# Kernel optimization log

Measured on AMD Instinct MI355X. Metric: run time of the kernel, lower is better.

Reference implementation:

```python
import jax, jax.numpy as jnp
import numpy as np

D = 512      # hidden_size
H = 8        # num_heads
EPS = 1e-5   # torch LayerNorm default eps


def _ln(x, g, b):
    m = x.mean(-1, keepdims=True)
    v = ((x - m) ** 2).mean(-1, keepdims=True)
    return (x - m) * jax.lax.rsqrt(v + EPS) * g + b


def _xavier(k, shape):
    fan_in, fan_out = shape
    lim = (6.0 / (fan_in + fan_out)) ** 0.5
    return jax.random.uniform(k, shape, jnp.float32, -lim, lim)


def setup_inputs() -> dict:
    key = jax.random.key(0)
    ks = jax.random.split(key, 8)
    lengths = np.array([512, 640, 768, 896, 1024, 512, 768, 1024], dtype=np.int64)
    cum = np.concatenate([np.zeros(1, np.int64), np.cumsum(lengths)])  # [9], last = 6144
    T = int(cum[-1])
    return {
        "h_n": jax.random.normal(ks[0], (T, D), jnp.float32),
        "to_v_w": _xavier(ks[1], (D, D)), "to_v_b": jnp.zeros((D,), jnp.float32),
        "to_qk_w": _xavier(ks[2], (D, 2 * D)), "to_qk_b": jnp.zeros((2 * D,), jnp.float32),
        "proj_w": _xavier(ks[3], (D, D)), "proj_b": jnp.zeros((D,), jnp.float32),
        "ffn_w1": _xavier(ks[4], (D, 4 * D)), "ffn_b1": jnp.zeros((4 * D,), jnp.float32),
        "ffn_w2": _xavier(ks[5], (4 * D, D)), "ffn_b2": jnp.zeros((D,), jnp.float32),
        "ln1_g": jnp.ones((D,), jnp.float32), "ln1_b": jnp.zeros((D,), jnp.float32),
        "ln2_g": jnp.ones((D,), jnp.float32), "ln2_b": jnp.zeros((D,), jnp.float32),
        "num_query_cumsum": jnp.asarray(cum),
    }


def reference(h_n, to_v_w, to_v_b, to_qk_w, to_qk_b, proj_w, proj_b,
              ffn_w1, ffn_b1, ffn_w2, ffn_b2, ln1_g, ln1_b, ln2_g, ln2_b,
              num_query_cumsum):
    # --- static ragged layout (indices are constants) ---
    cum = np.asarray(num_query_cumsum)
    lengths = np.diff(cum)                       # [B]
    B = int(lengths.size)
    N = int(lengths.max())                       # max_num_nodes
    T = int(cum[-1])
    bid = np.repeat(np.arange(B), lengths)       # [T] graph id per token
    pos = np.arange(T) - cum[bid]                # [T] slot within graph
    pad_mask = np.arange(N)[None, :] >= lengths[:, None]  # [B, N], True = padding

    hd = D // H
    scale = hd ** -0.5

    # --- projections on the flat ragged tokens ---
    v = h_n @ to_v_w + to_v_b                    # [T, D]
    qk = h_n @ to_qk_w + to_qk_b                 # [T, 2D]
    q, k = qk[:, :D], qk[:, D:]

    # --- pad ragged -> dense [B, H, N, hd] ---
    def pad(x):
        xp = jnp.zeros((B, N, D), x.dtype).at[bid, pos].set(x)
        return xp.reshape(B, N, H, hd).transpose(0, 2, 1, 3)

    qp, kp, vp = pad(q), pad(k), pad(v)

    # --- dense masked softmax attention (keys masked at pad slots) ---
    scores = jnp.einsum('bhnd,bhmd->bhnm', qp, kp) * scale
    scores = jnp.where(pad_mask[:, None, None, :], -jnp.inf, scores)
    attn = jax.nn.softmax(scores, axis=-1)
    ctx = jnp.einsum('bhnm,bhmd->bhnd', attn, vp)

    # --- unpad back to flat [T, D] ---
    h_new = ctx.transpose(0, 2, 1, 3).reshape(B, N, D)[bid, pos]

    # --- residual + LN + FFN + LN (dropout = 0) ---
    h1 = _ln(h_n + (h_new @ proj_w + proj_b), ln1_g, ln1_b)
    ffn = jax.nn.gelu(h1 @ ffn_w1 + ffn_b1, approximate=False) @ ffn_w2 + ffn_b2
    return _ln(h1 + ffn, ln2_g, ln2_b)
```

## Files before the change

kernel.cpp:

```cpp
#include <hip/hip_runtime.h>

typedef __bf16 bf16;
typedef __bf16 bf16x8 __attribute__((ext_vector_type(8)));
typedef __bf16 bf16x4 __attribute__((ext_vector_type(4)));
typedef float  f32x4  __attribute__((ext_vector_type(4)));

#define MFMA16 __builtin_amdgcn_mfma_f32_16x16x32_bf16

__device__ __forceinline__ void gl2lds16(const bf16* g, bf16* l) {
  __builtin_amdgcn_global_load_lds(
      (const __attribute__((address_space(1))) unsigned int*)g,
      (__attribute__((address_space(3))) unsigned int*)l, 16, 0, 0);
}

__device__ __forceinline__ int dt_bf16(const void* g1) {
  return (((const unsigned*)g1)[0] == 0x3F800000u) ? 0 : 1;
}
__device__ __forceinline__ float load_any(const void* p, int i, int f) {
  return f ? (float)((const bf16*)p)[i] : ((const float*)p)[i];
}

__global__ __launch_bounds__(256) void prep_all(
    const void* __restrict__ h, const void* __restrict__ w_qk,
    const void* __restrict__ w_v, const void* __restrict__ w_pr,
    const void* __restrict__ w_f1, const void* __restrict__ w_f2,
    const void* __restrict__ b_qk, const void* __restrict__ b_v,
    const void* __restrict__ b_pr, const void* __restrict__ b_f1,
    const void* __restrict__ b_f2, const void* __restrict__ g1,
    const void* __restrict__ b1, const void* __restrict__ g2,
    const void* __restrict__ b2,
    bf16* __restrict__ hb, bf16* __restrict__ Wtqkv, bf16* __restrict__ Wtpr,
    bf16* __restrict__ Wtf1, bf16* __restrict__ Wtf2,
    float* __restrict__ vec, int T) {
  __shared__ bf16 tile[32][33];
  const int f = dt_bf16(g1);
  const int t = threadIdx.x;
  int b = blockIdx.x;
  const int HB = (T * 512) / 2048;

  if (b < HB) {
    const int i = (b * 256 + t) * 8;
    if (f) {
      *(bf16x8*)&hb[i] = *(const bf16x8*)((const bf16*)h + i);
    } else {
      const float* hf = (const float*)h;
      bf16x8 v;
#pragma unroll
      for (int j = 0; j < 8; j++) v[j] = (bf16)hf[i + j];
      *(bf16x8*)&hb[i] = v;
    }
    return;
  }
  b -= HB;

  if (b < 3072) {
    const void* in; bf16* out; int K, N;
    if (b < 512)       { in = w_qk; out = Wtqkv;                     K = 512;  N = 1024; }
    else if (b < 768)  { b -= 512;  in = w_v;  out = Wtqkv + (size_t)1024 * 512; K = 512; N = 512; }
    else if (b < 1024) { b -= 768;  in = w_pr; out = Wtpr;           K = 512;  N = 512; }
    else if (b < 2048) { b -= 1024; in = w_f1; out = Wtf1;           K = 512;  N = 2048; }
    else               { b -= 2048; in = w_f2; out = Wtf2;           K = 2048; N = 512; }
    const int tilesx = N / 32;
    const int bx = (b % tilesx) * 32, by = (b / tilesx) * 32;
    const int tx = t & 31, ty = t >> 5;
#pragma unroll
    for (int i = 0; i < 32; i += 8)
      tile[ty + i][tx] = (bf16)load_any(in, (by + ty + i) * N + bx + tx, f);
    __syncthreads();
#pragma unroll
    for (int i = 0; i < 32; i += 8)
      out[(size_t)(bx + ty + i) * K + by + tx] = tile[tx][ty + i];
    return;
  }
  b -= 3072;

  const int i = b * 256 + t;
  if (i >= 6656) return;
  const void* src; int base;
  if (i < 1024)      { src = b_qk; base = 0; }
  else if (i < 1536) { src = b_v;  base = 1024; }
  else if (i < 2048) { src = b_pr; base = 1536; }
  else if (i < 4096) { src = b_f1; base = 2048; }
  else if (i < 4608) { src = b_f2; base = 4096; }
  else if (i < 5120) { src = g1;   base = 4608; }
  else if (i < 5632) { src = b1;   base = 5120; }
  else if (i < 6144) { src = g2;   base = 5632; }
  else               { src = b2;   base = 6144; }
  vec[i] = load_any(src, i - base, f);
}

template <int BM, int MODE>
__global__ __launch_bounds__(256) void gemm_lds(const bf16* __restrict__ A,
                                                const bf16* __restrict__ Bt,
                                                const float* __restrict__ bias,
                                                void* __restrict__ aux,
                                                void* __restrict__ outp,
                                                void* __restrict__ outp2,
                                                int N, int K, int ldA, int ldB,
                                                int ldT) {
  constexpr int BN = 128;
  constexpr int WAVES_M = BM / 64;
  constexpr int WAVES_N = 4 / WAVES_M;
  constexpr int WN = BN / WAVES_N;
  constexpr int NI = WN / 16;
  __shared__ __align__(16) bf16 As[BM * 64];
  __shared__ __align__(16) bf16 Bs[BN * 64];
  const int t = threadIdx.x;
  const int m0 = blockIdx.x * BM, n0 = blockIdx.y * BN;
  const int lane = t & 63, wv = t >> 6;
  const int wm = (wv / WAVES_N) * 64;
  const int wn = (wv % WAVES_N) * WN;
  const int qd = lane >> 4, cl = lane & 15;
  const int koff = (MODE == 6) ? blockIdx.z * K : 0;

  const f32x4 fz = {0.f, 0.f, 0.f, 0.f};
  f32x4 acc[4][NI];
#pragma unroll
  for (int i = 0; i < 4; i++)
#pragma unroll
    for (int j = 0; j < NI; j++) acc[i][j] = fz;

  const int srow = wv * 8 + (lane >> 3);
  const int sch = (lane & 7) ^ (lane >> 3);
  const bf16* pA = A + (size_t)(m0 + srow) * ldA + koff + sch * 8;
  const bf16* pB = Bt + (size_t)(n0 + srow) * ldB + koff + sch * 8;
  bf16* AsW = As + wv * 8 * 64;
  bf16* BsW = Bs + wv * 8 * 64;

  for (int k0 = 0; k0 < K; k0 += 64) {
    __syncthreads();
#pragma unroll
    for (int op = 0; op < BM / 32; op++)
      gl2lds16(pA + (size_t)(op * 32) * ldA, AsW + op * 32 * 64);
#pragma unroll
    for (int op = 0; op < 4; op++)
      gl2lds16(pB + (size_t)(op * 32) * ldB, BsW + op * 32 * 64);
    pA += 64; pB += 64;
    __syncthreads();

#pragma unroll
    for (int ss = 0; ss < 2; ss++) {
      bf16x8 af[4], bfr[NI];
#pragma unroll
      for (int i = 0; i < 4; i++)
        af[i] = *(const bf16x8*)&As[(wm + i * 16 + cl) * 64 +
                                    ((ss * 4 + qd) ^ (cl & 7)) * 8];
#pragma unroll
      for (int i = 0; i < NI; i++)
        bfr[i] = *(const bf16x8*)&Bs[(wn + i * 16 + cl) * 64 +
                                     ((ss * 4 + qd) ^ (cl & 7)) * 8];
#pragma unroll
      for (int mi = 0; mi < 4; mi++)
#pragma unroll
        for (int ni = 0; ni < NI; ni++)
          acc[mi][ni] = MFMA16(af[mi], bfr[ni], acc[mi][ni], 0, 0, 0);
    }
  }

  float bv[NI];
#pragma unroll
  for (int ni = 0; ni < NI; ni++)
    bv[ni] = (MODE == 6) ? 0.f : bias[n0 + wn + ni * 16 + cl];

#pragma unroll
  for (int mi = 0; mi < 4; mi++) {
    const int mbase = m0 + wm + mi * 16 + qd * 4;
#pragma unroll
    for (int ni = 0; ni < NI; ni++) {
      const int n = n0 + wn + ni * 16 + cl;
      if (MODE == 5) {
        if (n0 < 1024) {
          bf16* out = (bf16*)outp;
#pragma unroll
          for (int r = 0; r < 4; r++)
            out[(size_t)(mbase + r) * 1024 + n] = (bf16)(acc[mi][ni][r] + bv[ni]);
        } else {
          bf16* vtp = (bf16*)aux;
          bf16x4 pk;
#pragma unroll
          for (int r = 0; r < 4; r++) pk[r] = (bf16)(acc[mi][ni][r] + bv[ni]);
          *(bf16x4*)&vtp[(size_t)(n - 1024) * ldT + mbase] = pk;
        }
      } else if (MODE == 2) {
        float* out = (float*)outp;
        const bf16* res = (const bf16*)aux;
#pragma unroll
        for (int r = 0; r < 4; r++)
          out[(size_t)(mbase + r) * N + n] =
              acc[mi][ni][r] + bv[ni] + (float)res[(size_t)(mbase + r) * N + n];
      } else if (MODE == 3) {
        bf16* out = (bf16*)outp;
#pragma unroll
        for (int r = 0; r < 4; r++) {
          float x = acc[mi][ni][r] + bv[ni];
          float gl = 0.5f * x * (1.0f + erff(x * 0.70710678118654752f));
          out[(size_t)(mbase + r) * N + n] = (bf16)gl;
        }
      } else {
        float* out = (float*)(blockIdx.z ? outp2 : outp);
#pragma unroll
        for (int r = 0; r < 4; r++)
          out[(size_t)(mbase + r) * N + n] = acc[mi][ni][r];
      }
    }
  }
}

__global__ __launch_bounds__(256) void attn_kernel(const bf16* __restrict__ qk,
                                                   const bf16* __restrict__ vt,
                                                   bf16* __restrict__ ctx,
                                                   const int* __restrict__ cumraw,
                                                   int T, int ncum) {
  __shared__ __align__(16) bf16 Ks[2][64 * 64];
  __shared__ __align__(16) bf16 Vs[2][64 * 64];
  __shared__ __align__(16) bf16 P[4][16 * 64];
  const int wv = threadIdx.x >> 6, lane = threadIdx.x & 63;
  const int qd = lane >> 4, cl = lane & 15;
  const int q0b = blockIdx.x * 64;
  const int q0 = q0b + wv * 16;
  const int h = blockIdx.y;

  const int stride = (cumraw[1] == 0) ? 2 : 1;
  int kstart = 0, kend = T;
  for (int i = 1; i < ncum; i++) {
    int c = cumraw[i * stride];
    if (c > q0b) { kend = c; break; }
    kstart = c;
  }

  const bf16* qbase = qk + (size_t)(q0 + cl) * 1024 + h * 64 + qd * 8;
  bf16x8 qf0 = *(const bf16x8*)qbase;
  bf16x8 qf1 = *(const bf16x8*)(qbase + 32);

  const f32x4 fz = {0.f, 0.f, 0.f, 0.f};
  f32x4 o[4] = {fz, fz, fz, fz};
  float lacc[4] = {0.f, 0.f, 0.f, 0.f};

  const int srow = wv * 8 + (lane >> 3);
  const int schunk = (lane & 7) ^ (srow & 7);
  const bf16* kg = qk + 512 + (size_t)h * 64 + schunk * 8;
  const bf16* vg = vt + (size_t)(h * 64 + srow) * T + schunk * 8;
  const int woff = wv * 8 * 64;

  const int bch = qd ^ (cl & 7);
  const float cc = 0.1803368801111204f;

  {
    const bf16* kg0 = kg + (size_t)(kstart + srow) * 1024;
    gl2lds16(kg0, Ks[0] + woff);
    gl2lds16(kg0 + (size_t)32 * 1024, Ks[0] + woff + 32 * 64);
    const bf16* vg0 = vg + kstart;
    gl2lds16(vg0, Vs[0] + woff);
    gl2lds16(vg0 + (size_t)32 * T, Vs[0] + woff + 32 * 64);
  }

  int ib = 0;
  for (int kc = kstart; kc < kend; kc += 64, ib ^= 1) {
    __syncthreads();

    if (kc + 64 < kend) {
      const bf16* kg0 = kg + (size_t)(kc + 64 + srow) * 1024;
      gl2lds16(kg0, Ks[ib ^ 1] + woff);
      gl2lds16(kg0 + (size_t)32 * 1024, Ks[ib ^ 1] + woff + 32 * 64);
      const bf16* vg0 = vg + kc + 64;
      gl2lds16(vg0, Vs[ib ^ 1] + woff);
      gl2lds16(vg0 + (size_t)32 * T, Vs[ib ^ 1] + woff + 32 * 64);
    }

    f32x4 s[4];
#pragma unroll
    for (int ni = 0; ni < 4; ni++) {
      const bf16* kr = Ks[ib] + (ni * 16 + cl) * 64;
      f32x4 tacc = fz;
      tacc = MFMA16(qf0, *(const bf16x8*)(kr + bch * 8), tacc, 0, 0, 0);
      tacc = MFMA16(qf1, *(const bf16x8*)(kr + (bch ^ 4) * 8), tacc, 0, 0, 0);
      s[ni] = tacc;
    }

    bf16* Pw = P[wv];
#pragma unroll
    for (int r = 0; r < 4; r++) {
      const float p0 = __builtin_amdgcn_exp2f(s[0][r] * cc);
      const float p1 = __builtin_amdgcn_exp2f(s[1][r] * cc);
      const float p2 = __builtin_amdgcn_exp2f(s[2][r] * cc);
      const float p3 = __builtin_amdgcn_exp2f(s[3][r] * cc);
      lacc[r] += (p0 + p1) + (p2 + p3);
      const int prow = qd * 4 + r;
      const int px = prow & 7;
      const int cb = cl >> 3, ci = cl & 7;
      Pw[prow * 64 + ((cb ^ px) * 8) + ci] = (bf16)p0;
      Pw[prow * 64 + (((2 + cb) ^ px) * 8) + ci] = (bf16)p1;
      Pw[prow * 64 + (((4 + cb) ^ px) * 8) + ci] = (bf16)p2;
      Pw[prow * 64 + (((6 + cb) ^ px) * 8) + ci] = (bf16)p3;
    }

    const int pch = qd ^ (cl & 7);
    const bf16* pr = Pw + cl * 64;
    bf16x8 pf0 = *(const bf16x8*)(pr + pch * 8);
    bf16x8 pf1 = *(const bf16x8*)(pr + (pch ^ 4) * 8);
#pragma unroll
    for (int dt = 0; dt < 4; dt++) {
      const bf16* vr = Vs[ib] + (dt * 16 + cl) * 64;
      o[dt] = MFMA16(pf0, *(const bf16x8*)(vr + bch * 8), o[dt], 0, 0, 0);
      o[dt] = MFMA16(pf1, *(const bf16x8*)(vr + (bch ^ 4) * 8), o[dt], 0, 0, 0);
    }
  }

  float linv[4];
#pragma unroll
  for (int r = 0; r < 4; r++) {
    float l = lacc[r];
    l += __shfl_xor(l, 1);
    l += __shfl_xor(l, 2);
    l += __shfl_xor(l, 4);
    l += __shfl_xor(l, 8);
    linv[r] = __builtin_amdgcn_rcpf(l);
  }
#pragma unroll
  for (int dt = 0; dt < 4; dt++) {
#pragma unroll
    for (int r = 0; r < 4; r++) {
      float y = o[dt][r] * linv[r];
      ctx[(size_t)(q0 + qd * 4 + r) * 512 + h * 64 + dt * 16 + cl] = (bf16)y;
    }
  }
}

__global__ __launch_bounds__(256) void ln_kernel(const float* __restrict__ s,
                                                 const float* __restrict__ g,
                                                 const float* __restrict__ b,
                                                 bf16* __restrict__ outb) {
  const int row = blockIdx.x * 4 + (threadIdx.x >> 6);
  const int lane = threadIdx.x & 63;
  const float4* sr = (const float4*)(s + (size_t)row * 512);
  float4 x0 = sr[lane];
  float4 x1 = sr[lane + 64];
  float sum = x0.x + x0.y + x0.z + x0.w + x1.x + x1.y + x1.z + x1.w;
  float sq = x0.x * x0.x + x0.y * x0.y + x0.z * x0.z + x0.w * x0.w +
             x1.x * x1.x + x1.y * x1.y + x1.z * x1.z + x1.w * x1.w;
#pragma unroll
  for (int off = 1; off < 64; off <<= 1) {
    sum += __shfl_xor(sum, off);
    sq += __shfl_xor(sq, off);
  }
  const float mean = sum * (1.0f / 512.0f);
  const float var = sq * (1.0f / 512.0f) - mean * mean;
  const float rs = rsqrtf(var + 1e-5f);
  const float4* gp = (const float4*)g;
  const float4* bp = (const float4*)b;
  float4 g0 = gp[lane], g1v = gp[lane + 64];
  float4 b0 = bp[lane], b1v = bp[lane + 64];
  float xv[8] = {x0.x, x0.y, x0.z, x0.w, x1.x, x1.y, x1.z, x1.w};
  float gv[8] = {g0.x, g0.y, g0.z, g0.w, g1v.x, g1v.y, g1v.z, g1v.w};
  float bb[8] = {b0.x, b0.y, b0.z, b0.w, b1v.x, b1v.y, b1v.z, b1v.w};
  bf16x4 o0, o1;
#pragma unroll
  for (int j = 0; j < 4; j++) {
    o0[j] = (bf16)((xv[j] - mean) * rs * gv[j] + bb[j]);
    o1[j] = (bf16)((xv[4 + j] - mean) * rs * gv[4 + j] + bb[4 + j]);
  }
  *(bf16x4*)&outb[(size_t)row * 512 + lane * 4] = o0;
  *(bf16x4*)&outb[(size_t)row * 512 + 256 + lane * 4] = o1;
}

__global__ __launch_bounds__(256) void ln2_kernel(const float* __restrict__ s2a,
                                                  const float* __restrict__ s2b,
                                                  const bf16* __restrict__ h1b,
                                                  const float* __restrict__ bias,
                                                  const float* __restrict__ g,
                                                  const float* __restrict__ b,
                                                  void* __restrict__ outb,
                                                  const void* __restrict__ g1probe) {
  const int row = blockIdx.x * 4 + (threadIdx.x >> 6);
  const int lane = threadIdx.x & 63;
  const float4* sa = (const float4*)(s2a + (size_t)row * 512);
  const float4* sb = (const float4*)(s2b + (size_t)row * 512);
  const float4* bi = (const float4*)bias;
  float4 a0 = sa[lane], a1 = sa[lane + 64];
  float4 c0 = sb[lane], c1 = sb[lane + 64];
  float4 v0 = bi[lane], v1 = bi[lane + 64];
  bf16x4 h0 = *(const bf16x4*)&h1b[(size_t)row * 512 + lane * 4];
  bf16x4 h1 = *(const bf16x4*)&h1b[(size_t)row * 512 + 256 + lane * 4];
  float x[8];
#pragma unroll
  for (int j = 0; j < 4; j++) {
    x[j] = (&a0.x)[j] + (&c0.x)[j] + (&v0.x)[j] + (float)h0[j];
    x[4 + j] = (&a1.x)[j] + (&c1.x)[j] + (&v1.x)[j] + (float)h1[j];
  }
  float sum = 0.f, sq = 0.f;
#pragma unroll
  for (int j = 0; j < 8; j++) { sum += x[j]; sq += x[j] * x[j]; }
#pragma unroll
  for (int off = 1; off < 64; off <<= 1) {
    sum += __shfl_xor(sum, off);
    sq += __shfl_xor(sq, off);
  }
  const float mean = sum * (1.0f / 512.0f);
  const float var = sq * (1.0f / 512.0f) - mean * mean;
  const float rs = rsqrtf(var + 1e-5f);
  const float4* gp = (const float4*)g;
  const float4* bp = (const float4*)b;
  float4 g0 = gp[lane], g1v = gp[lane + 64];
  float4 b0 = bp[lane], b1v = bp[lane + 64];
  float gv[8] = {g0.x, g0.y, g0.z, g0.w, g1v.x, g1v.y, g1v.z, g1v.w};
  float bb[8] = {b0.x, b0.y, b0.z, b0.w, b1v.x, b1v.y, b1v.z, b1v.w};
  float y[8];
#pragma unroll
  for (int j = 0; j < 8; j++) y[j] = (x[j] - mean) * rs * gv[j] + bb[j];

  if (dt_bf16(g1probe)) {
    bf16* ob = (bf16*)outb;
    bf16x4 o0, o1;
#pragma unroll
    for (int j = 0; j < 4; j++) { o0[j] = (bf16)y[j]; o1[j] = (bf16)y[4 + j]; }
    *(bf16x4*)&ob[(size_t)row * 512 + lane * 4] = o0;
    *(bf16x4*)&ob[(size_t)row * 512 + 256 + lane * 4] = o1;
  } else {
    float4* of = (float4*)((float*)outb + (size_t)row * 512);
    of[lane] = make_float4(y[0], y[1], y[2], y[3]);
    of[lane + 64] = make_float4(y[4], y[5], y[6], y[7]);
  }
}

extern "C" void kernel_launch(void* const* d_in, const int* in_sizes, int n_in,
                              void* d_out, int out_size, void* d_ws, size_t ws_size,
                              hipStream_t stream) {
  (void)n_in; (void)out_size; (void)ws_size;
  const void* h_n  = d_in[0];
  const void* w_v  = d_in[1];
  const void* b_v  = d_in[2];
  const void* w_qk = d_in[3];
  const void* b_qk = d_in[4];
  const void* w_pr = d_in[5];
  const void* b_pr = d_in[6];
  const void* w_f1 = d_in[7];
  const void* b_f1 = d_in[8];
  const void* w_f2 = d_in[9];
  const void* b_f2 = d_in[10];
  const void* g1w  = d_in[11];
  const void* b1w  = d_in[12];
  const void* g2w  = d_in[13];
  const void* b2w  = d_in[14];
  const int* cum   = (const int*)d_in[15];
  const int T = in_sizes[0] / 512;
  const int ncum = in_sizes[15];

  char* ws = (char*)d_ws;
  size_t off = 0;
  auto alloc = [&](size_t bytes) {
    char* p = ws + off;
    off += (bytes + 255) & ~(size_t)255;
    return p;
  };
  float* vec = (float*)alloc(6656 * 4);
  bf16* hb   = (bf16*)alloc((size_t)T * 512 * 2);
  bf16* qkb  = (bf16*)alloc((size_t)T * 1024 * 2);
  bf16* vt   = (bf16*)alloc((size_t)T * 512 * 2);
  bf16* ctx  = (bf16*)alloc((size_t)T * 512 * 2);
  float* s1  = (float*)alloc((size_t)T * 512 * 4);
  bf16* h1b  = (bf16*)alloc((size_t)T * 512 * 2);
  float* s2b = (float*)alloc((size_t)T * 512 * 4);
  bf16* Wtqkv = (bf16*)alloc((size_t)1536 * 512 * 2);
  bf16* Wtpr  = (bf16*)alloc((size_t)512 * 512 * 2);
  bf16* Wtf1  = (bf16*)alloc((size_t)2048 * 512 * 2);
  bf16* Wtf2  = (bf16*)alloc((size_t)512 * 2048 * 2);
  bf16* gbuf = qkb;
  float* s2a = s1;

  float* fb_qkv = vec + 0;
  float* fb_pr  = vec + 1536;
  float* fb_f1  = vec + 2048;
  float* fb_f2  = vec + 4096;
  float* fg1 = vec + 4608, *fb1 = vec + 5120;
  float* fg2 = vec + 5632, *fb2 = vec + 6144;

  const int prep_blocks = (T * 512) / 2048 + 3072 + 26;
  prep_all<<<prep_blocks, 256, 0, stream>>>(
      h_n, w_qk, w_v, w_pr, w_f1, w_f2,
      b_qk, b_v, b_pr, b_f1, b_f2, g1w, b1w, g2w, b2w,
      hb, Wtqkv, Wtpr, Wtf1, Wtf2, vec, T);

  gemm_lds<128, 5><<<dim3(T / 128, 12), 256, 0, stream>>>(
      hb, Wtqkv, fb_qkv, vt, qkb, nullptr, 1536, 512, 512, 512, T);
  attn_kernel<<<dim3(T / 64, 8), 256, 0, stream>>>(qkb, vt, ctx, cum, T, ncum);
  gemm_lds<64, 2><<<dim3(T / 64, 4), 256, 0, stream>>>(
      ctx, Wtpr, fb_pr, (void*)hb, s1, nullptr, 512, 512, 512, 512, 0);
  ln_kernel<<<T / 4, 256, 0, stream>>>(s1, fg1, fb1, h1b);
  gemm_lds<128, 3><<<dim3(T / 128, 16), 256, 0, stream>>>(
      h1b, Wtf1, fb_f1, nullptr, gbuf, nullptr, 2048, 512, 512, 512, 0);
  gemm_lds<128, 6><<<dim3(T / 128, 4, 2), 256, 0, stream>>>(
      gbuf, Wtf2, nullptr, nullptr, s2a, s2b, 512, 1024, 2048, 2048, 0);
  ln2_kernel<<<T / 4, 256, 0, stream>>>(s2a, s2b, h1b, fb_f2, fg2, fb2, d_out, g1w);
}
```

Baseline: 219.4 us.

## Process 32 queries per wave in attention; drop split-K for FFN2 GEMM

The attention kernel now gives each wave 32 query rows (two 16-row tiles) and each block 128 queries. Every K/V fragment read from LDS therefore feeds twice as many MFMAs, and the block count halves. Blocks that straddle a graph boundary load the union of key ranges, and each wave skips chunks outside its own graph. The FFN down-projection drops its split-K with two fp32 partial outputs and instead uses a single 64-row GEMM that fuses bias and residual, so ln2 reads only one buffer. The cost is fewer attention blocks, fewer FFN2 blocks with a longer K loop, and wasted K/V loads on boundary-straddling blocks.

```diff
diff --git a/kernel.cpp b/kernel.cpp
--- a/kernel.cpp
+++ b/kernel.cpp
@@ -95,7 +95,6 @@
                                                 const float* __restrict__ bias,
                                                 void* __restrict__ aux,
                                                 void* __restrict__ outp,
-                                                void* __restrict__ outp2,
                                                 int N, int K, int ldA, int ldB,
                                                 int ldT) {
   constexpr int BN = 128;
@@ -111,7 +110,6 @@
   const int wm = (wv / WAVES_N) * 64;
   const int wn = (wv % WAVES_N) * WN;
   const int qd = lane >> 4, cl = lane & 15;
-  const int koff = (MODE == 6) ? blockIdx.z * K : 0;
 
   const f32x4 fz = {0.f, 0.f, 0.f, 0.f};
   f32x4 acc[4][NI];
@@ -122,8 +120,8 @@
 
   const int srow = wv * 8 + (lane >> 3);
   const int sch = (lane & 7) ^ (lane >> 3);
-  const bf16* pA = A + (size_t)(m0 + srow) * ldA + koff + sch * 8;
-  const bf16* pB = Bt + (size_t)(n0 + srow) * ldB + koff + sch * 8;
+  const bf16* pA = A + (size_t)(m0 + srow) * ldA + sch * 8;
+  const bf16* pB = Bt + (size_t)(n0 + srow) * ldB + sch * 8;
   bf16* AsW = As + wv * 8 * 64;
   bf16* BsW = Bs + wv * 8 * 64;
 
@@ -159,8 +157,7 @@
 
   float bv[NI];
 #pragma unroll
-  for (int ni = 0; ni < NI; ni++)
-    bv[ni] = (MODE == 6) ? 0.f : bias[n0 + wn + ni * 16 + cl];
+  for (int ni = 0; ni < NI; ni++) bv[ni] = bias[n0 + wn + ni * 16 + cl];
 
 #pragma unroll
   for (int mi = 0; mi < 4; mi++) {
@@ -188,7 +185,7 @@
         for (int r = 0; r < 4; r++)
           out[(size_t)(mbase + r) * N + n] =
               acc[mi][ni][r] + bv[ni] + (float)res[(size_t)(mbase + r) * N + n];
-      } else if (MODE == 3) {
+      } else {
         bf16* out = (bf16*)outp;
 #pragma unroll
         for (int r = 0; r < 4; r++) {
@@ -196,11 +193,6 @@
           float gl = 0.5f * x * (1.0f + erff(x * 0.70710678118654752f));
           out[(size_t)(mbase + r) * N + n] = (bf16)gl;
         }
-      } else {
-        float* out = (float*)(blockIdx.z ? outp2 : outp);
-#pragma unroll
-        for (int r = 0; r < 4; r++)
-          out[(size_t)(mbase + r) * N + n] = acc[mi][ni][r];
       }
     }
   }
@@ -213,28 +205,42 @@
                                                    int T, int ncum) {
   __shared__ __align__(16) bf16 Ks[2][64 * 64];
   __shared__ __align__(16) bf16 Vs[2][64 * 64];
-  __shared__ __align__(16) bf16 P[4][16 * 64];
+  __shared__ __align__(16) bf16 P[4][32 * 64];
   const int wv = threadIdx.x >> 6, lane = threadIdx.x & 63;
   const int qd = lane >> 4, cl = lane & 15;
-  const int q0b = blockIdx.x * 64;
-  const int q0 = q0b + wv * 16;
+  const int q0b = blockIdx.x * 128;
+  const int q0w = q0b + wv * 32;
   const int h = blockIdx.y;
 
   const int stride = (cumraw[1] == 0) ? 2 : 1;
-  int kstart = 0, kend = T;
+  int ks_w = 0, ke_w = T;
   for (int i = 1; i < ncum; i++) {
     int c = cumraw[i * stride];
-    if (c > q0b) { kend = c; break; }
-    kstart = c;
-  }
-
-  const bf16* qbase = qk + (size_t)(q0 + cl) * 1024 + h * 64 + qd * 8;
-  bf16x8 qf0 = *(const bf16x8*)qbase;
-  bf16x8 qf1 = *(const bf16x8*)(qbase + 32);
+    if (c > q0w) { ke_w = c; break; }
+    ks_w = c;
+  }
+  int ks_u = 0, ke_u = T;
+  for (int i = 1; i < ncum; i++) {
+    int c = cumraw[i * stride];
+    if (c > q0b) { ke_u = c; break; }
+    ks_u = c;
+  }
+  for (int i = 1; i < ncum; i++) {
+    int c = cumraw[i * stride];
+    if (c > q0b + 127) { ke_u = c; break; }
+  }
+
+  bf16x8 qf[2][2];
+#pragma unroll
+  for (int a = 0; a < 2; a++) {
+    const bf16* qb = qk + (size_t)(q0w + a * 16 + cl) * 1024 + h * 64 + qd * 8;
+    qf[a][0] = *(const bf16x8*)qb;
+    qf[a][1] = *(const bf16x8*)(qb + 32);
+  }
 
   const f32x4 fz = {0.f, 0.f, 0.f, 0.f};
-  f32x4 o[4] = {fz, fz, fz, fz};
-  float lacc[4] = {0.f, 0.f, 0.f, 0.f};
+  f32x4 o[2][4] = {{fz, fz, fz, fz}, {fz, fz, fz, fz}};
+  float lacc[2][4] = {{0.f, 0.f, 0.f, 0.f}, {0.f, 0.f, 0.f, 0.f}};
 
   const int srow = wv * 8 + (lane >> 3);
   const int schunk = (lane & 7) ^ (srow & 7);
@@ -246,19 +252,19 @@
   const float cc = 0.1803368801111204f;
 
   {
-    const bf16* kg0 = kg + (size_t)(kstart + srow) * 1024;
+    const bf16* kg0 = kg + (size_t)(ks_u + srow) * 1024;
     gl2lds16(kg0, Ks[0] + woff);
     gl2lds16(kg0 + (size_t)32 * 1024, Ks[0] + woff + 32 * 64);
-    const bf16* vg0 = vg + kstart;
+    const bf16* vg0 = vg + ks_u;
     gl2lds16(vg0, Vs[0] + woff);
     gl2lds16(vg0 + (size_t)32 * T, Vs[0] + woff + 32 * 64);
   }
 
   int ib = 0;
-  for (int kc = kstart; kc < kend; kc += 64, ib ^= 1) {
+  for (int kc = ks_u; kc < ke_u; kc += 64, ib ^= 1) {
     __syncthreads();
 
-    if (kc + 64 < kend) {
+    if (kc + 64 < ke_u) {
       const bf16* kg0 = kg + (size_t)(kc + 64 + srow) * 1024;
       gl2lds16(kg0, Ks[ib ^ 1] + woff);
       gl2lds16(kg0 + (size_t)32 * 1024, Ks[ib ^ 1] + woff + 32 * 64);
@@ -267,61 +273,81 @@
       gl2lds16(vg0 + (size_t)32 * T, Vs[ib ^ 1] + woff + 32 * 64);
     }
 
-    f32x4 s[4];
-#pragma unroll
-    for (int ni = 0; ni < 4; ni++) {
-      const bf16* kr = Ks[ib] + (ni * 16 + cl) * 64;
-      f32x4 tacc = fz;
-      tacc = MFMA16(qf0, *(const bf16x8*)(kr + bch * 8), tacc, 0, 0, 0);
-      tacc = MFMA16(qf1, *(const bf16x8*)(kr + (bch ^ 4) * 8), tacc, 0, 0, 0);
-      s[ni] = tacc;
+    if (kc >= ks_w && kc < ke_w) {
+      f32x4 s[2][4];
+#pragma unroll
+      for (int ni = 0; ni < 4; ni++) {
+        const bf16* kr = Ks[ib] + (ni * 16 + cl) * 64;
+        bf16x8 k0 = *(const bf16x8*)(kr + bch * 8);
+        bf16x8 k1 = *(const bf16x8*)(kr + (bch ^ 4) * 8);
+#pragma unroll
+        for (int a = 0; a < 2; a++) {
+          f32x4 ta = fz;
+          ta = MFMA16(qf[a][0], k0, ta, 0, 0, 0);
+          ta = MFMA16(qf[a][1], k1, ta, 0, 0, 0);
+          s[a][ni] = ta;
+        }
+      }
+
+      bf16* Pw = P[wv];
+#pragma unroll
+      for (int a = 0; a < 2; a++) {
+        bf16* Pa = Pw + a * 16 * 64;
+#pragma unroll
+        for (int r = 0; r < 4; r++) {
+          const float p0 = __builtin_amdgcn_exp2f(s[a][0][r] * cc);
+          const float p1 = __builtin_amdgcn_exp2f(s[a][1][r] * cc);
+          const float p2 = __builtin_amdgcn_exp2f(s[a][2][r] * cc);
+          const float p3 = __builtin_amdgcn_exp2f(s[a][3][r] * cc);
+          lacc[a][r] += (p0 + p1) + (p2 + p3);
+          const int prow = qd * 4 + r;
+          const int px = prow & 7;
+          const int cb = cl >> 3, ci = cl & 7;
+          Pa[prow * 64 + ((cb ^ px) * 8) + ci] = (bf16)p0;
+          Pa[prow * 64 + (((2 + cb) ^ px) * 8) + ci] = (bf16)p1;
+          Pa[prow * 64 + (((4 + cb) ^ px) * 8) + ci] = (bf16)p2;
+          Pa[prow * 64 + (((6 + cb) ^ px) * 8) + ci] = (bf16)p3;
+        }
+      }
+
+      const int pch = qd ^ (cl & 7);
+      bf16x8 pf[2][2];
+#pragma unroll
+      for (int a = 0; a < 2; a++) {
+        const bf16* pr = Pw + a * 16 * 64 + cl * 64;
+        pf[a][0] = *(const bf16x8*)(pr + pch * 8);
+        pf[a][1] = *(const bf16x8*)(pr + (pch ^ 4) * 8);
+      }
+#pragma unroll
+      for (int dt = 0; dt < 4; dt++) {
+        const bf16* vr = Vs[ib] + (dt * 16 + cl) * 64;
+        bf16x8 v0 = *(const bf16x8*)(vr + bch * 8);
+        bf16x8 v1 = *(const bf16x8*)(vr + (bch ^ 4) * 8);
+#pragma unroll
+        for (int a = 0; a < 2; a++) {
+          o[a][dt] = MFMA16(pf[a][0], v0, o[a][dt], 0, 0, 0);
+          o[a][dt] = MFMA16(pf[a][1], v1, o[a][dt], 0, 0, 0);
+        }
+      }
     }
-
-    bf16* Pw = P[wv];
+  }
+
+#pragma unroll
+  for (int a = 0; a < 2; a++) {
 #pragma unroll
     for (int r = 0; r < 4; r++) {
-      const float p0 = __builtin_amdgcn_exp2f(s[0][r] * cc);
-      const float p1 = __builtin_amdgcn_exp2f(s[1][r] * cc);
-      const float p2 = __builtin_amdgcn_exp2f(s[2][r] * cc);
-      const float p3 = __builtin_amdgcn_exp2f(s[3][r] * cc);
-      lacc[r] += (p0 + p1) + (p2 + p3);
-      const int prow = qd * 4 + r;
-      const int px = prow & 7;
-      const int cb = cl >> 3, ci = cl & 7;
-      Pw[prow * 64 + ((cb ^ px) * 8) + ci] = (bf16)p0;
-      Pw[prow * 64 + (((2 + cb) ^ px) * 8) + ci] = (bf16)p1;
-      Pw[prow * 64 + (((4 + cb) ^ px) * 8) + ci] = (bf16)p2;
-      Pw[prow * 64 + (((6 + cb) ^ px) * 8) + ci] = (bf16)p3;
-    }
-
-    const int pch = qd ^ (cl & 7);
-    const bf16* pr = Pw + cl * 64;
-    bf16x8 pf0 = *(const bf16x8*)(pr + pch * 8);
-    bf16x8 pf1 = *(const bf16x8*)(pr + (pch ^ 4) * 8);
-#pragma unroll
-    for (int dt = 0; dt < 4; dt++) {
-      const bf16* vr = Vs[ib] + (dt * 16 + cl) * 64;
-      o[dt] = MFMA16(pf0, *(const bf16x8*)(vr + bch * 8), o[dt], 0, 0, 0);
-      o[dt] = MFMA16(pf1, *(const bf16x8*)(vr + (bch ^ 4) * 8), o[dt], 0, 0, 0);
-    }
-  }
-
-  float linv[4];
-#pragma unroll
-  for (int r = 0; r < 4; r++) {
-    float l = lacc[r];
-    l += __shfl_xor(l, 1);
-    l += __shfl_xor(l, 2);
-    l += __shfl_xor(l, 4);
-    l += __shfl_xor(l, 8);
-    linv[r] = __builtin_amdgcn_rcpf(l);
-  }
-#pragma unroll
-  for (int dt = 0; dt < 4; dt++) {
-#pragma unroll
-    for (int r = 0; r < 4; r++) {
-      float y = o[dt][r] * linv[r];
-      ctx[(size_t)(q0 + qd * 4 + r) * 512 + h * 64 + dt * 16 + cl] = (bf16)y;
+      float l = lacc[a][r];
+      l += __shfl_xor(l, 1);
+      l += __shfl_xor(l, 2);
+      l += __shfl_xor(l, 4);
+      l += __shfl_xor(l, 8);
+      const float li = __builtin_amdgcn_rcpf(l);
+#pragma unroll
+      for (int dt = 0; dt < 4; dt++) {
+        float y = o[a][dt][r] * li;
+        ctx[(size_t)(q0w + a * 16 + qd * 4 + r) * 512 + h * 64 + dt * 16 + cl] =
+            (bf16)y;
+      }
     }
   }
 }
@@ -363,33 +389,19 @@
   *(bf16x4*)&outb[(size_t)row * 512 + 256 + lane * 4] = o1;
 }
 
-__global__ __launch_bounds__(256) void ln2_kernel(const float* __restrict__ s2a,
-                                                  const float* __restrict__ s2b,
-                                                  const bf16* __restrict__ h1b,
-                                                  const float* __restrict__ bias,
+__global__ __launch_bounds__(256) void ln2_kernel(const float* __restrict__ s,
                                                   const float* __restrict__ g,
                                                   const float* __restrict__ b,
                                                   void* __restrict__ outb,
                                                   const void* __restrict__ g1probe) {
   const int row = blockIdx.x * 4 + (threadIdx.x >> 6);
   const int lane = threadIdx.x & 63;
-  const float4* sa = (const float4*)(s2a + (size_t)row * 512);
-  const float4* sb = (const float4*)(s2b + (size_t)row * 512);
-  const float4* bi = (const float4*)bias;
-  float4 a0 = sa[lane], a1 = sa[lane + 64];
-  float4 c0 = sb[lane], c1 = sb[lane + 64];
-  float4 v0 = bi[lane], v1 = bi[lane + 64];
-  bf16x4 h0 = *(const bf16x4*)&h1b[(size_t)row * 512 + lane * 4];
-  bf16x4 h1 = *(const bf16x4*)&h1b[(size_t)row * 512 + 256 + lane * 4];
-  float x[8];
-#pragma unroll
-  for (int j = 0; j < 4; j++) {
-    x[j] = (&a0.x)[j] + (&c0.x)[j] + (&v0.x)[j] + (float)h0[j];
-    x[4 + j] = (&a1.x)[j] + (&c1.x)[j] + (&v1.x)[j] + (float)h1[j];
-  }
-  float sum = 0.f, sq = 0.f;
-#pragma unroll
-  for (int j = 0; j < 8; j++) { sum += x[j]; sq += x[j] * x[j]; }
+  const float4* sr = (const float4*)(s + (size_t)row * 512);
+  float4 x0 = sr[lane];
+  float4 x1 = sr[lane + 64];
+  float sum = x0.x + x0.y + x0.z + x0.w + x1.x + x1.y + x1.z + x1.w;
+  float sq = x0.x * x0.x + x0.y * x0.y + x0.z * x0.z + x0.w * x0.w +
+             x1.x * x1.x + x1.y * x1.y + x1.z * x1.z + x1.w * x1.w;
 #pragma unroll
   for (int off = 1; off < 64; off <<= 1) {
     sum += __shfl_xor(sum, off);
@@ -402,11 +414,12 @@
   const float4* bp = (const float4*)b;
   float4 g0 = gp[lane], g1v = gp[lane + 64];
   float4 b0 = bp[lane], b1v = bp[lane + 64];
+  float xv[8] = {x0.x, x0.y, x0.z, x0.w, x1.x, x1.y, x1.z, x1.w};
   float gv[8] = {g0.x, g0.y, g0.z, g0.w, g1v.x, g1v.y, g1v.z, g1v.w};
   float bb[8] = {b0.x, b0.y, b0.z, b0.w, b1v.x, b1v.y, b1v.z, b1v.w};
   float y[8];
 #pragma unroll
-  for (int j = 0; j < 8; j++) y[j] = (x[j] - mean) * rs * gv[j] + bb[j];
+  for (int j = 0; j < 8; j++) y[j] = (xv[j] - mean) * rs * gv[j] + bb[j];
 
   if (dt_bf16(g1probe)) {
     bf16* ob = (bf16*)outb;
@@ -459,13 +472,12 @@
   bf16* ctx  = (bf16*)alloc((size_t)T * 512 * 2);
   float* s1  = (float*)alloc((size_t)T * 512 * 4);
   bf16* h1b  = (bf16*)alloc((size_t)T * 512 * 2);
-  float* s2b = (float*)alloc((size_t)T * 512 * 4);
   bf16* Wtqkv = (bf16*)alloc((size_t)1536 * 512 * 2);
   bf16* Wtpr  = (bf16*)alloc((size_t)512 * 512 * 2);
   bf16* Wtf1  = (bf16*)alloc((size_t)2048 * 512 * 2);
   bf16* Wtf2  = (bf16*)alloc((size_t)512 * 2048 * 2);
   bf16* gbuf = qkb;
-  float* s2a = s1;
+  float* s2 = s1;
 
   float* fb_qkv = vec + 0;
   float* fb_pr  = vec + 1536;
@@ -481,14 +493,14 @@
       hb, Wtqkv, Wtpr, Wtf1, Wtf2, vec, T);
 
   gemm_lds<128, 5><<<dim3(T / 128, 12), 256, 0, stream>>>(
-      hb, Wtqkv, fb_qkv, vt, qkb, nullptr, 1536, 512, 512, 512, T);
-  attn_kernel<<<dim3(T / 64, 8), 256, 0, stream>>>(qkb, vt, ctx, cum, T, ncum);
+      hb, Wtqkv, fb_qkv, vt, qkb, 1536, 512, 512, 512, T);
+  attn_kernel<<<dim3(T / 128, 8), 256, 0, stream>>>(qkb, vt, ctx, cum, T, ncum);
   gemm_lds<64, 2><<<dim3(T / 64, 4), 256, 0, stream>>>(
-      ctx, Wtpr, fb_pr, (void*)hb, s1, nullptr, 512, 512, 512, 512, 0);
+      ctx, Wtpr, fb_pr, (void*)hb, s1, 512, 512, 512, 512, 0);
   ln_kernel<<<T / 4, 256, 0, stream>>>(s1, fg1, fb1, h1b);
   gemm_lds<128, 3><<<dim3(T / 128, 16), 256, 0, stream>>>(
-      h1b, Wtf1, fb_f1, nullptr, gbuf, nullptr, 2048, 512, 512, 512, 0);
-  gemm_lds<128, 6><<<dim3(T / 128, 4, 2), 256, 0, stream>>>(
-      gbuf, Wtf2, nullptr, nullptr, s2a, s2b, 512, 1024, 2048, 2048, 0);
-  ln2_kernel<<<T / 4, 256, 0, stream>>>(s2a, s2b, h1b, fb_f2, fg2, fb2, d_out, g1w);
-}
+      h1b, Wtf1, fb_f1, nullptr, gbuf, 2048, 512, 512, 512, 0);
+  gemm_lds<64, 2><<<dim3(T / 64, 4), 256, 0, stream>>>(
+      gbuf, Wtf2, fb_f2, (void*)h1b, s2, 512, 2048, 2048, 2048, 0);
+  ln2_kernel<<<T / 4, 256, 0, stream>>>(s2, fg2, fb2, d_out, g1w);
+}
```

Measured after the change: 236.1 us. 1.08x slower.
